# Kernel optimization log

Measured on AMD Instinct MI355X. Metric: run time of the kernel, lower is better.

Reference implementation:

```python
import jax, jax.numpy as jnp
import numpy as np
from functools import partial

SIGMA = 0.1       # blend_params.sigma (heaviside noise intensity)
GAMMA = 0.1       # blend_params.gamma (argmax noise intensity / z softening)
ZNEAR = 1.0
ZFAR = 100.0
NB_SAMPLES = 4
EPS = 1e-10
N, H, W, K = 8, 256, 256, 8


def random_heaviside(x, noise, sigma):
    # x: (N,H,W,K), noise: (S,N,H,W,K). torch.heaviside(v, ones): 1 for v>=0 else 0.
    maps = (x + sigma * noise >= 0).astype(x.dtype)
    return maps.mean(axis=0)


def random_argmax(z, noise, gamma):
    # z: (N,H,W,Kp), noise: (S,N,H,W,Kp). One-hot of per-sample argmax, averaged.
    zp = z + gamma * noise
    w = jax.nn.one_hot(jnp.argmax(zp, axis=-1), z.shape[-1], dtype=z.dtype)
    return w.mean(axis=0)


def reference(colors, dists, zbuf, pix_to_face, background):
    kh, ka = jax.random.split(jax.random.key(1))
    noise_h = jax.random.normal(kh, (NB_SAMPLES, N, H, W, K), dtype=colors.dtype)
    noise_a = jax.random.normal(ka, (NB_SAMPLES, N, H, W, K + 1), dtype=colors.dtype)

    mask = (pix_to_face >= 0).astype(colors.dtype)          # (N,H,W,K)
    prob_map = random_heaviside(-dists, noise_h, SIGMA) * mask
    alpha = jnp.prod(1.0 - prob_map, axis=-1)               # (N,H,W)

    z_inv = (ZFAR - zbuf) / (ZFAR - ZNEAR) * mask
    z_inv_max = jnp.clip(jnp.max(z_inv, axis=-1, keepdims=True), EPS)
    z_map = jnp.log(EPS + prob_map) + (z_inv - z_inv_max) / GAMMA
    bg_score = jnp.broadcast_to((EPS - z_inv_max) / GAMMA, z_map.shape[:-1] + (1,))
    z_map = jnp.concatenate([z_map, bg_score], axis=-1)     # (N,H,W,K+1)

    randomax = random_argmax(z_map, noise_a, GAMMA)
    wz, wb = randomax[..., :-1], randomax[..., -1:]
    weighted_colors = jnp.einsum('nhwk,nhwkc->nhwc', wz, colors)
    rgb = weighted_colors + wb * background                 # (N,H,W,3)
    a = (1.0 - alpha)[..., None]
    return jnp.concatenate([rgb, a], axis=-1)               # (N,H,W,4)


def setup_inputs() -> dict:
    key = jax.random.key(0)
    k1, k2, k3, k4 = jax.random.split(key, 4)
    colors = jax.random.normal(k1, (N, H, W, K, 3), dtype=jnp.float32)
    dists = jax.random.normal(k2, (N, H, W, K), dtype=jnp.float32)
    zbuf = jax.random.uniform(k3, (N, H, W, K), dtype=jnp.float32)
    pix_to_face = jax.random.randint(k4, (N, H, W, K), 0, 1000)
    background = jnp.ones((3,), dtype=jnp.float32)
    return {"colors": colors, "dists": dists, "zbuf": zbuf,
            "pix_to_face": pix_to_face, "background": background}
```

## Files before the change

kernel.cpp:

```cpp
#include <hip/hip_runtime.h>
#include <cstdint>
#include <cmath>


#pragma clang fp contract(off)

#define NPIX 524288
#define STRIDE_H 4194304u
#define STRIDE_A 4718592u
#define BAND_A 5e-5f

__device__ __forceinline__ uint32_t rotl32(uint32_t v, int n) {
  return (v << n) | (v >> (32 - n));
}

__device__ __forceinline__ void tf2x32(uint32_t k0, uint32_t k1,
                                       uint32_t c0, uint32_t c1,
                                       uint32_t& o0, uint32_t& o1) {
  const uint32_t k2 = k0 ^ k1 ^ 0x1BD11BDAu;
  uint32_t x0 = c0 + k0, x1 = c1 + k1;
#define TFR(r) { x0 += x1; x1 = rotl32(x1, r); x1 ^= x0; }
  TFR(13) TFR(15) TFR(26) TFR(6)
  x0 += k1;  x1 += k2 + 1u;
  TFR(17) TFR(29) TFR(16) TFR(24)
  x0 += k2;  x1 += k0 + 2u;
  TFR(13) TFR(15) TFR(26) TFR(6)
  x0 += k0;  x1 += k1 + 3u;
  TFR(17) TFR(29) TFR(16) TFR(24)
  x0 += k1;  x1 += k2 + 4u;
  TFR(13) TFR(15) TFR(26) TFR(6)
  x0 += k2;  x1 += k0 + 5u;
#undef TFR
  o0 = x0; o1 = x1;
}

__device__ __forceinline__ double fast_log(double z) {
  uint64_t b = __double_as_longlong(z);
  int E = (int)(b >> 52) - 1023;
  double m = __longlong_as_double((b & 0x000FFFFFFFFFFFFFULL) |
                                  0x3FF0000000000000ULL);
  bool c = m > 1.4142135623730951;
  m = c ? m * 0.5 : m;
  E = c ? E + 1 : E;
  double d = m + 1.0;
  double r = __builtin_amdgcn_rcp(d);
  r = fma(r, fma(-d, r, 1.0), r);
  r = fma(r, fma(-d, r, 1.0), r);
  double s = (m - 1.0) * r;
  double u = s * s;
  double p = 1.0 / 19.0;
  p = fma(p, u, 1.0 / 17.0);
  p = fma(p, u, 1.0 / 15.0);
  p = fma(p, u, 1.0 / 13.0);
  p = fma(p, u, 1.0 / 11.0);
  p = fma(p, u, 1.0 / 9.0);
  p = fma(p, u, 1.0 / 7.0);
  p = fma(p, u, 1.0 / 5.0);
  p = fma(p, u, 1.0 / 3.0);
  p = fma(p, u, 1.0);
  double lm = (2.0 * s) * p;
  const double LN2_HI = 6.93147180369123816490e-01;
  const double LN2_LO = 1.90821492927058770002e-10;
  double e = (double)E;
  return fma(e, LN2_HI, fma(e, LN2_LO, lm));
}

__device__ __forceinline__ float normal_exact(uint32_t bits) {
  float f = __uint_as_float((bits >> 9) | 0x3f800000u) - 1.0f;
  const float lo = __uint_as_float(0xBF7FFFFFu);
  float v = __fadd_rn(__fmul_rn(f, 2.0f), lo);
  v = fmaxf(lo, v);
  float t = -__fmul_rn(v, v);
  float taylor = __fmul_rn(__fadd_rn(__fmul_rn(-0.5f, t), 1.0f), t);
  float lg = (float)fast_log((double)__fadd_rn(t, 1.0f));
  float l1p = (fabsf(t) < 1e-4f) ? taylor : lg;
  float w = -l1p;
  const bool lt = w < 5.0f;
  float ww = lt ? __fsub_rn(w, 2.5f) : __fsub_rn(__fsqrt_rn(w), 3.0f);
  float p  = lt ? 2.81022636e-08f : -0.000200214257f;
  p = __fadd_rn(lt ?  3.43273939e-07f :  0.000100950558f, __fmul_rn(p, ww));
  p = __fadd_rn(lt ? -3.5233877e-06f  :  0.00134934322f,  __fmul_rn(p, ww));
  p = __fadd_rn(lt ? -4.39150654e-06f : -0.00367342844f,  __fmul_rn(p, ww));
  p = __fadd_rn(lt ?  0.00021858087f  :  0.00573950773f,  __fmul_rn(p, ww));
  p = __fadd_rn(lt ? -0.00125372503f  : -0.0076224613f,   __fmul_rn(p, ww));
  p = __fadd_rn(lt ? -0.00417768164f  :  0.00943887047f,  __fmul_rn(p, ww));
  p = __fadd_rn(lt ?  0.246640727f    :  1.00167406f,     __fmul_rn(p, ww));
  p = __fadd_rn(lt ?  1.50140941f     :  2.83297682f,     __fmul_rn(p, ww));
  return __fmul_rn(__uint_as_float(0x3FB504F3u), __fmul_rn(p, v));
}

__device__ __forceinline__ float score_fast(uint32_t bits, float zmj) {
  float f = __uint_as_float((bits >> 9) | 0x3f800000u) - 1.0f;
  const float lo = __uint_as_float(0xBF7FFFFFu);
  float v = fmaxf(lo, __fmaf_rn(f, 2.0f, lo));
  float t = -__fmul_rn(v, v);
  float u = __fadd_rn(t, 1.0f);
  float L = __builtin_amdgcn_logf(u);
  float ww = __fmaf_rn(-0.69314718f, L, -2.5f);
  float p = 2.81022636e-08f;
  p = __fmaf_rn(p, ww,  3.43273939e-07f);
  p = __fmaf_rn(p, ww, -3.5233877e-06f);
  p = __fmaf_rn(p, ww, -4.39150654e-06f);
  p = __fmaf_rn(p, ww,  0.00021858087f);
  p = __fmaf_rn(p, ww, -0.00125372503f);
  p = __fmaf_rn(p, ww, -0.00417768164f);
  p = __fmaf_rn(p, ww,  0.246640727f);
  p = __fmaf_rn(p, ww,  1.50140941f);
  if (__builtin_expect(__ballot(L <= -7.2134752f) != 0ull, 0)) {
    float w = __fmul_rn(-0.69314718f, L);
    float w2 = __builtin_amdgcn_sqrtf(w) - 3.0f;
    float q = -0.000200214257f;
    q = __fmaf_rn(q, w2,  0.000100950558f);
    q = __fmaf_rn(q, w2,  0.00134934322f);
    q = __fmaf_rn(q, w2, -0.00367342844f);
    q = __fmaf_rn(q, w2,  0.00573950773f);
    q = __fmaf_rn(q, w2, -0.0076224613f);
    q = __fmaf_rn(q, w2,  0.00943887047f);
    q = __fmaf_rn(q, w2,  1.00167406f);
    q = __fmaf_rn(q, w2,  2.83297682f);
    p = (L <= -7.2134752f) ? q : p;
  }
  return __fmaf_rn(__fmul_rn(p, v), 0.14142136f, zmj);
}

__global__ __launch_bounds__(256) void RandomPhongShader_kernel(
    const float* __restrict__ colors,
    const float* __restrict__ dists,
    const float* __restrict__ zbuf,
    const int*   __restrict__ p2f,
    const float* __restrict__ bg,
    float* __restrict__ out)
{
  __shared__ float zmS[256][9];
  const int tid = threadIdx.x;
  const int P = blockIdx.x * 256 + tid;

  uint32_t kh0, kh1, ka0, ka1;
  tf2x32(0u, 1u, 0u, 0u, kh0, kh1);
  tf2x32(0u, 1u, 0u, 1u, ka0, ka1);

  int Tm6[8];
  {
    const float4* d4 = reinterpret_cast<const float4*>(dists + (size_t)P * 8);
    float4 a = d4[0], b = d4[1];
    float dk[8] = {a.x,a.y,a.z,a.w,b.x,b.y,b.z,b.w};
    #pragma unroll
    for (int k = 0; k < 8; ++k) {
      float y = fabsf(dk[k]) * 7.0710678f;
      float tt = __builtin_amdgcn_rcpf(__fmaf_rn(0.3275911f, y, 1.0f));
      float ex = __builtin_amdgcn_exp2f(__fmul_rn(-1.4426951f, y * y));
      float pp = 1.061405429f;
      pp = __fmaf_rn(pp, tt, -1.453152027f);
      pp = __fmaf_rn(pp, tt,  1.421413741f);
      pp = __fmaf_rn(pp, tt, -0.284496736f);
      pp = __fmaf_rn(pp, tt,  0.254829592f);
      float er = __fmaf_rn(-pp * tt, ex, 1.0f);
      float vs = copysignf(er, dk[k]);
      int T = (int)ceilf(__fmul_rn(__fadd_rn(vs, 0.99999994f), 4194304.0f));
      Tm6[k] = T - 6;
    }
  }

  uint32_t cntP = 0;
  bool redoH = false;
  {
    uint32_t cH = (uint32_t)P * 8u;
    #pragma unroll 1
    for (int s = 0; s < 4; ++s) {
      #pragma unroll
      for (int k = 0; k < 8; ++k) {
        uint32_t o0, o1;
        tf2x32(kh0, kh1, 0u, cH + (uint32_t)k, o0, o1);
        int m = (int)((o0 ^ o1) >> 9);
        int sub = m - Tm6[k];
        cntP += (sub >= 6) ? (1u << (4 * k)) : 0u;
        redoH |= ((uint32_t)sub <= 12u);
      }
      cH += STRIDE_H;
    }
  }
  if (__builtin_expect(__ballot(redoH) != 0ull, 0)) {
    if (redoH) {
      uint32_t c2 = 0;
      #pragma unroll 1
      for (int i = 0; i < 32; ++i) {
        uint32_t s = (uint32_t)i >> 3, k = (uint32_t)i & 7u;
        uint32_t o0, o1;
        tf2x32(kh0, kh1, 0u, s * STRIDE_H + (uint32_t)P * 8u + k, o0, o1);
        float nz = normal_exact(o0 ^ o1);
        float x = -dists[(size_t)P * 8 + k];
        c2 += (__fadd_rn(x, __fmul_rn(0.1f, nz)) >= 0.0f) ? (1u << (4 * k)) : 0u;
      }
      cntP = c2;
    }
  }

  uint32_t msk;
  {
    const int4* m4 = reinterpret_cast<const int4*>(p2f + (size_t)P * 8);
    int4 f = m4[0], g = m4[1];
    msk  = (f.x >= 0 ? 1u : 0u) | (f.y >= 0 ? 2u : 0u)
         | (f.z >= 0 ? 4u : 0u) | (f.w >= 0 ? 8u : 0u)
         | (g.x >= 0 ? 16u : 0u) | (g.y >= 0 ? 32u : 0u)
         | (g.z >= 0 ? 64u : 0u) | (g.w >= 0 ? 128u : 0u);
  }
  float zinv[8], zmax;
  {
    const float4* z4 = reinterpret_cast<const float4*>(zbuf + (size_t)P * 8);
    float4 c = z4[0], e = z4[1];
    float zk[8] = {c.x,c.y,c.z,c.w,e.x,e.y,e.z,e.w};
    #pragma unroll
    for (int k = 0; k < 8; ++k) {
      const float m = ((msk >> k) & 1u) ? 1.0f : 0.0f;
      float zi = __fmul_rn(__fdiv_rn(__fsub_rn(100.0f, zk[k]), 99.0f), m);
      zinv[k] = zi;
      zmax = (k == 0) ? zi : fmaxf(zmax, zi);
    }
  }
  zmax = fmaxf(zmax, 1e-10f);

  const float lg0 = (float)-23.025850916589025;
  const float lg1 = (float)-1.3862943611198906;
  const float lg2 = (float)-0.6931471805599453;
  const float lg3 = (float)-0.2876820724517809;

  float alpha = 1.0f;
  float zm[9];
  #pragma unroll
  for (int k = 0; k < 8; ++k) {
    const int cntk = (int)((cntP >> (4 * k)) & 15u);
    const bool mb = ((msk >> k) & 1u) != 0u;
    const float pm = mb ? __fmul_rn((float)cntk, 0.25f) : 0.0f;
    alpha *= (1.0f - pm);
    const int i = mb ? cntk : 0;
    const float lg = (i == 0) ? lg0 : (i == 1) ? lg1 : (i == 2) ? lg2
                   : (i == 3) ? lg3 : 0.0f;
    zm[k] = __fadd_rn(lg, __fdiv_rn(__fsub_rn(zinv[k], zmax), 0.1f));
    zmS[tid][k] = zm[k];
  }
  zm[8] = __fdiv_rn(__fsub_rn(1e-10f, zmax), 0.1f);
  zmS[tid][8] = zm[8];

  uint32_t amPack = 0;
  uint32_t cA = (uint32_t)P * 9u;
  #pragma unroll 1
  for (int s = 0; s < 4; ++s) {
    int am = 0;
    float best = -3.4e38f, second = -3.4e38f;
    #pragma unroll
    for (int j = 0; j < 9; ++j) {
      uint32_t o0, o1;
      tf2x32(ka0, ka1, 0u, cA + (uint32_t)j, o0, o1);
      float vv = score_fast(o0 ^ o1, zm[j]);
      bool g = vv > best;
      second = g ? best : fmaxf(second, vv);
      best = g ? vv : best;
      am = g ? j : am;
    }
    bool fl = __fsub_rn(best, second) < BAND_A;
    if (__builtin_expect(__ballot(fl) != 0ull, 0)) {
      if (fl) {
        int ame = 0;
        float be = -3.4e38f;
        #pragma unroll 1
        for (int j = 0; j < 9; ++j) {
          uint32_t o0, o1;
          tf2x32(ka0, ka1, 0u, cA + (uint32_t)j, o0, o1);
          float nz = normal_exact(o0 ^ o1);
          float ve = __fadd_rn(zmS[tid][j], __fmul_rn(0.1f, nz));
          bool g = ve > be;
          be = g ? ve : be;
          ame = g ? j : ame;
        }
        am = ame;
      }
    }
    amPack += 1u << (3 * am);
    cA += STRIDE_A;
  }

  float rgb[3] = {0.0f, 0.0f, 0.0f};
  {
    const float4* c4 = reinterpret_cast<const float4*>(colors + (size_t)P * 24);
    float cc[24];
    #pragma unroll
    for (int q = 0; q < 6; ++q) {
      float4 t = c4[q];
      cc[q*4+0]=t.x; cc[q*4+1]=t.y; cc[q*4+2]=t.z; cc[q*4+3]=t.w;
    }
    #pragma unroll
    for (int c = 0; c < 3; ++c) {
      float acc = 0.0f;
      #pragma unroll
      for (int k = 0; k < 8; ++k) {
        float wk = __fmul_rn(0.25f, (float)((amPack >> (3 * k)) & 7u));
        acc = __fadd_rn(acc, __fmul_rn(wk, cc[k * 3 + c]));
      }
      float wb = __fmul_rn(0.25f, (float)((amPack >> 24) & 7u));
      rgb[c] = __fadd_rn(acc, __fmul_rn(wb, bg[c]));
    }
  }

  float4 o;
  o.x = rgb[0]; o.y = rgb[1]; o.z = rgb[2];
  o.w = __fsub_rn(1.0f, alpha);
  reinterpret_cast<float4*>(out)[P] = o;
}

extern "C" void kernel_launch(void* const* d_in, const int* in_sizes, int n_in,
                              void* d_out, int out_size, void* d_ws, size_t ws_size,
                              hipStream_t stream) {
  const float* colors = (const float*)d_in[0];
  const float* dists  = (const float*)d_in[1];
  const float* zbuf   = (const float*)d_in[2];
  const int*   p2f    = (const int*)d_in[3];
  const float* bg     = (const float*)d_in[4];
  float* out = (float*)d_out;
  dim3 grid(NPIX / 256), block(256);
  hipLaunchKernelGGL(RandomPhongShader_kernel, grid, block, 0, stream,
                     colors, dists, zbuf, p2f, bg, out);
}
```

Baseline: 191.3 us.

## Compact undecided elements per wave and skip provably decided RNG draws

Heaviside draws are skipped for entries with |dist| ≥ 0.55, since the bounded noise cannot flip the sign there. The remaining (pixel, k) entries are compacted into a per-wave LDS list so all lanes stay busy generating threefry samples. For the random argmax, candidates more than 1.10 below the best softened score are dropped as unable to win. Surviving candidates are compacted the same way, and top-1/top-2 scores are reduced through LDS 64-bit and 32-bit atomicMax, with the exact fallback kept for near ties. This aims to cut most of the threefry and score work, at the cost of extra LDS traffic, block barriers and atomics, and correctness depends on the noise magnitude bounds implied by the thresholds.

```diff
diff --git a/kernel.cpp b/kernel.cpp
--- a/kernel.cpp
+++ b/kernel.cpp
@@ -9,6 +9,8 @@
 #define STRIDE_H 4194304u
 #define STRIDE_A 4718592u
 #define BAND_A 5e-5f
+#define DET_THR 0.55f
+#define ELIM_THR 1.10f
 
 __device__ __forceinline__ uint32_t rotl32(uint32_t v, int n) {
   return (v << n) | (v >> (32 - n));
@@ -123,6 +125,28 @@
   return __fmaf_rn(__fmul_rn(p, v), 0.14142136f, zmj);
 }
 
+__device__ __forceinline__ uint32_t map_f32(float s) {
+  uint32_t u = __float_as_uint(s);
+  return u ^ ((uint32_t)((int32_t)u >> 31) | 0x80000000u);
+}
+__device__ __forceinline__ float unmap_f32(uint32_t m) {
+  uint32_t u = m ^ ((uint32_t)((int32_t)(~m) >> 31) | 0x80000000u);
+  return __uint_as_float(u);
+}
+
+__device__ __forceinline__ int wave_exscan4(int v, int& total) {
+  int pre = 0; total = 0;
+  #pragma unroll
+  for (int b = 0; b < 4; ++b) {
+    unsigned long long bl = __ballot(((v >> b) & 1) != 0);
+    int below = (int)__builtin_amdgcn_mbcnt_hi(
+        (uint32_t)(bl >> 32), __builtin_amdgcn_mbcnt_lo((uint32_t)bl, 0u));
+    pre += below << b;
+    total += (int)__popcll(bl) << b;
+  }
+  return pre;
+}
+
 __global__ __launch_bounds__(256) void RandomPhongShader_kernel(
     const float* __restrict__ colors,
     const float* __restrict__ dists,
@@ -131,19 +155,32 @@
     const float* __restrict__ bg,
     float* __restrict__ out)
 {
+  union SlotU {
+    int T[256][8];
+    unsigned long long s1[4][256];
+  };
+  __shared__ SlotU SU;
+  __shared__ unsigned int S2[4][256];
   __shared__ float zmS[256][9];
-  const int tid = threadIdx.x;
-  const int P = blockIdx.x * 256 + tid;
+  __shared__ __align__(8) unsigned char cntS[256][8];
+  __shared__ unsigned short listS[4][576];
+
+  const int tid  = threadIdx.x;
+  const int lane = tid & 63;
+  const int wv   = tid >> 6;
+  const int P    = blockIdx.x * 256 + tid;
+  const int Pw   = blockIdx.x * 256 + (wv << 6);
 
   uint32_t kh0, kh1, ka0, ka1;
   tf2x32(0u, 1u, 0u, 0u, kh0, kh1);
   tf2x32(0u, 1u, 0u, 1u, ka0, ka1);
 
-  int Tm6[8];
+  uint32_t ndm = 0, p4m = 0;
   {
     const float4* d4 = reinterpret_cast<const float4*>(dists + (size_t)P * 8);
     float4 a = d4[0], b = d4[1];
     float dk[8] = {a.x,a.y,a.z,a.w,b.x,b.y,b.z,b.w};
+    int t8[8];
     #pragma unroll
     for (int k = 0; k < 8; ++k) {
       float y = fabsf(dk[k]) * 7.0710678f;
@@ -157,43 +194,66 @@
       float er = __fmaf_rn(-pp * tt, ex, 1.0f);
       float vs = copysignf(er, dk[k]);
       int T = (int)ceilf(__fmul_rn(__fadd_rn(vs, 0.99999994f), 4194304.0f));
-      Tm6[k] = T - 6;
-    }
-  }
-
-  uint32_t cntP = 0;
-  bool redoH = false;
-  {
-    uint32_t cH = (uint32_t)P * 8u;
+      t8[k] = T - 6;
+      ndm |= (fabsf(dk[k]) < DET_THR) ? (1u << k) : 0u;
+      p4m |= (dk[k] <= -DET_THR) ? (1u << k) : 0u;
+    }
+    int4* tp = reinterpret_cast<int4*>(&SU.T[tid][0]);
+    tp[0] = make_int4(t8[0], t8[1], t8[2], t8[3]);
+    tp[1] = make_int4(t8[4], t8[5], t8[6], t8[7]);
+  }
+
+  int Wtot;
+  {
+    int off = wave_exscan4(__builtin_popcount(ndm), Wtot);
+    uint32_t m = ndm;
+    int idx = off;
+    while (m) {
+      int k = __builtin_ctz(m); m &= m - 1;
+      listS[wv][idx++] = (unsigned short)((lane << 3) | k);
+    }
+  }
+  __syncthreads();
+
+  {
+    const int trips = (Wtot + 63) >> 6;
     #pragma unroll 1
-    for (int s = 0; s < 4; ++s) {
+    for (int t = 0; t < trips; ++t) {
+      const int i = (t << 6) + lane;
+      const bool valid = i < Wtot;
+      const unsigned short itm = listS[wv][valid ? i : 0];
+      const int ow = itm >> 3, k = itm & 7;
+      const int oTid = (wv << 6) | ow;
+      const int To = SU.T[oTid][k];
+      const uint32_t base = (uint32_t)(Pw + ow) * 8u + (uint32_t)k;
+      uint32_t cnt = 0; bool band = false;
       #pragma unroll
-      for (int k = 0; k < 8; ++k) {
+      for (int s = 0; s < 4; ++s) {
         uint32_t o0, o1;
-        tf2x32(kh0, kh1, 0u, cH + (uint32_t)k, o0, o1);
-        int m = (int)((o0 ^ o1) >> 9);
-        int sub = m - Tm6[k];
-        cntP += (sub >= 6) ? (1u << (4 * k)) : 0u;
-        redoH |= ((uint32_t)sub <= 12u);
+        tf2x32(kh0, kh1, 0u, base + (uint32_t)s * STRIDE_H, o0, o1);
+        int mm = (int)((o0 ^ o1) >> 9);
+        int sub = mm - To;
+        cnt += (sub >= 6) ? 1u : 0u;
+        band |= ((uint32_t)sub <= 12u);
       }
-      cH += STRIDE_H;
-    }
-  }
-  if (__builtin_expect(__ballot(redoH) != 0ull, 0)) {
-    if (redoH) {
-      uint32_t c2 = 0;
-      #pragma unroll 1
-      for (int i = 0; i < 32; ++i) {
-        uint32_t s = (uint32_t)i >> 3, k = (uint32_t)i & 7u;
-        uint32_t o0, o1;
-        tf2x32(kh0, kh1, 0u, s * STRIDE_H + (uint32_t)P * 8u + k, o0, o1);
-        float nz = normal_exact(o0 ^ o1);
-        float x = -dists[(size_t)P * 8 + k];
-        c2 += (__fadd_rn(x, __fmul_rn(0.1f, nz)) >= 0.0f) ? (1u << (4 * k)) : 0u;
+      if (__builtin_expect(__ballot(band && valid) != 0ull, 0)) {
+        if (band && valid) {
+          float x = -dists[(size_t)base];
+          uint32_t c2 = 0;
+          #pragma unroll 1
+          for (int s = 0; s < 4; ++s) {
+            uint32_t o0, o1;
+            tf2x32(kh0, kh1, 0u, base + (uint32_t)s * STRIDE_H, o0, o1);
+            float nz = normal_exact(o0 ^ o1);
+            c2 += (__fadd_rn(x, __fmul_rn(0.1f, nz)) >= 0.0f) ? 1u : 0u;
+          }
+          cnt = c2;
+        }
       }
-      cntP = c2;
-    }
-  }
+      if (valid) cntS[oTid][k] = (unsigned char)cnt;
+    }
+  }
+  __syncthreads();
 
   uint32_t msk;
   {
@@ -224,11 +284,14 @@
   const float lg2 = (float)-0.6931471805599453;
   const float lg3 = (float)-0.2876820724517809;
 
+  const uint2 cg = *reinterpret_cast<const uint2*>(&cntS[tid][0]);
   float alpha = 1.0f;
   float zm[9];
   #pragma unroll
   for (int k = 0; k < 8; ++k) {
-    const int cntk = (int)((cntP >> (4 * k)) & 15u);
+    const uint32_t byte_ = ((k < 4 ? cg.x : cg.y) >> (8 * (k & 3))) & 0xffu;
+    const int cntk = ((ndm >> k) & 1u) ? (int)byte_
+                    : ((((p4m >> k) & 1u) != 0u) ? 4 : 0);
     const bool mb = ((msk >> k) & 1u) != 0u;
     const float pm = mb ? __fmul_rn((float)cntk, 0.25f) : 0.0f;
     alpha *= (1.0f - pm);
@@ -241,23 +304,71 @@
   zm[8] = __fdiv_rn(__fsub_rn(1e-10f, zmax), 0.1f);
   zmS[tid][8] = zm[8];
 
+  float bz = zm[0];
+  #pragma unroll
+  for (int j = 1; j < 9; ++j) bz = fmaxf(bz, zm[j]);
+  const float thr = __fsub_rn(bz, ELIM_THR);
+  uint32_t vm = 0;
+  #pragma unroll
+  for (int j = 0; j < 9; ++j) vm |= (zm[j] >= thr) ? (1u << j) : 0u;
+  const int V  = __builtin_popcount(vm);
+  const int j0 = __builtin_ctz(vm);
+
+  int W3;
+  {
+    int off3 = wave_exscan4((V >= 2) ? V : 0, W3);
+    uint32_t m = (V >= 2) ? vm : 0u;
+    int idx = off3;
+    while (m) {
+      int j = __builtin_ctz(m); m &= m - 1;
+      listS[wv][idx++] = (unsigned short)((lane << 4) | j);
+    }
+  }
+  #pragma unroll
+  for (int s = 0; s < 4; ++s) { SU.s1[s][tid] = 0ull; S2[s][tid] = 0u; }
+  __syncthreads();
+
+  const int trips3 = (W3 + 63) >> 6;
+  #pragma unroll 1
+  for (int t = 0; t < trips3; ++t) {
+    const int i = (t << 6) + lane;
+    const bool valid = i < W3;
+    const unsigned short itm = listS[wv][valid ? i : 0];
+    const int ow = itm >> 4, j = itm & 15;
+    const int oTid = (wv << 6) | ow;
+    const float zo = zmS[oTid][j];
+    const uint32_t cb3 = (uint32_t)(Pw + ow) * 9u + (uint32_t)j;
+    const unsigned long long jtag = (unsigned long long)(15 - j);
+    #pragma unroll
+    for (int s = 0; s < 4; ++s) {
+      uint32_t o0, o1;
+      tf2x32(ka0, ka1, 0u, cb3 + (uint32_t)s * STRIDE_A, o0, o1);
+      float sc = score_fast(o0 ^ o1, zo);
+      unsigned long long key = ((unsigned long long)map_f32(sc) << 32) | jtag;
+      if (valid) {
+        unsigned long long old = atomicMax(&SU.s1[s][oTid], key);
+        unsigned long long mn = key < old ? key : old;
+        atomicMax(&S2[s][oTid], (unsigned int)(mn >> 32));
+      }
+    }
+  }
+  __syncthreads();
+
   uint32_t amPack = 0;
-  uint32_t cA = (uint32_t)P * 9u;
+  const uint32_t cAo = (uint32_t)P * 9u;
   #pragma unroll 1
   for (int s = 0; s < 4; ++s) {
-    int am = 0;
-    float best = -3.4e38f, second = -3.4e38f;
-    #pragma unroll
-    for (int j = 0; j < 9; ++j) {
-      uint32_t o0, o1;
-      tf2x32(ka0, ka1, 0u, cA + (uint32_t)j, o0, o1);
-      float vv = score_fast(o0 ^ o1, zm[j]);
-      bool g = vv > best;
-      second = g ? best : fmaxf(second, vv);
-      best = g ? vv : best;
-      am = g ? j : am;
-    }
-    bool fl = __fsub_rn(best, second) < BAND_A;
+    int js;
+    bool fl = false;
+    if (V >= 2) {
+      const unsigned long long b1 = SU.s1[s][tid];
+      js = 15 - (int)(b1 & 0xFFFFu);
+      const float s1f = unmap_f32((uint32_t)(b1 >> 32));
+      const float s2f = unmap_f32(S2[s][tid]);
+      fl = __fsub_rn(s1f, s2f) < BAND_A;
+    } else {
+      js = j0;
+    }
     if (__builtin_expect(__ballot(fl) != 0ull, 0)) {
       if (fl) {
         int ame = 0;
@@ -265,18 +376,18 @@
         #pragma unroll 1
         for (int j = 0; j < 9; ++j) {
           uint32_t o0, o1;
-          tf2x32(ka0, ka1, 0u, cA + (uint32_t)j, o0, o1);
+          tf2x32(ka0, ka1, 0u, cAo + (uint32_t)s * STRIDE_A + (uint32_t)j,
+                 o0, o1);
           float nz = normal_exact(o0 ^ o1);
           float ve = __fadd_rn(zmS[tid][j], __fmul_rn(0.1f, nz));
           bool g = ve > be;
           be = g ? ve : be;
           ame = g ? j : ame;
         }
-        am = ame;
+        js = ame;
       }
     }
-    amPack += 1u << (3 * am);
-    cA += STRIDE_A;
+    amPack += 1u << (3 * js);
   }
 
   float rgb[3] = {0.0f, 0.0f, 0.0f};
```

Result: faster. 169.0 us (-11.7%).
